# Performance work log

Hardware: AMD Instinct MI355X
Metric: run time of the kernel (lower is better)

Reference implementation:

```python
import jax, jax.numpy as jnp
import numpy as np

D_MODEL = 1024
NHEAD = 16
D_K = D_MODEL // NHEAD
MAX_REL = 1024


def setup_inputs() -> dict:
    key = jax.random.key(0)
    ks = jax.random.split(key, 6)
    B, S = 4, 2048
    s = 1.0 / np.sqrt(D_MODEL)
    x = jax.random.normal(ks[0], (B, S, D_MODEL), dtype=jnp.float32)
    W_qkv = jax.random.normal(ks[1], (D_MODEL, 3 * D_MODEL), dtype=jnp.float32) * s
    b_qkv = jnp.zeros((3 * D_MODEL,), dtype=jnp.float32)
    W_out = jax.random.normal(ks[2], (D_MODEL, D_MODEL), dtype=jnp.float32) * s
    b_out = jnp.zeros((D_MODEL,), dtype=jnp.float32)
    # torch init is zeros; use small random so bias path is exercised
    rel_bias = jax.random.normal(ks[3], (2 * MAX_REL + 1, NHEAD), dtype=jnp.float32) * 0.02
    return {"x": x, "W_qkv": W_qkv, "b_qkv": b_qkv, "W_out": W_out,
            "b_out": b_out, "rel_bias": rel_bias}


def reference(x, W_qkv, b_qkv, W_out, b_out, rel_bias):
    B, S, D = x.shape
    qkv = x @ W_qkv + b_qkv                      # [B,S,3D]
    qkv = qkv.reshape(B, S, 3, NHEAD, D_K)
    q, k, v = qkv[:, :, 0], qkv[:, :, 1], qkv[:, :, 2]  # [B,S,H,dk]
    # scores: [B,H,S,S]
    scores = jnp.einsum('bihd,bjhd->bhij', q, k) / jnp.sqrt(jnp.float32(D_K))
    idxs = jnp.arange(S)
    rel = jnp.clip(idxs[:, None] - idxs[None, :] + MAX_REL, 0, 2 * MAX_REL)  # [S,S]
    bias = rel_bias[rel]                         # [S,S,H]
    scores = scores + jnp.transpose(bias, (2, 0, 1))[None]  # broadcast over batch
    attn = jax.nn.softmax(scores, axis=-1)       # dropout p=0 (eval)
    out = jnp.einsum('bhij,bjhd->bihd', attn, v).reshape(B, S, D)
    return out @ W_out + b_out
```

## Files before the change

### kernel.cpp

```cpp
#include <hip/hip_runtime.h>

#define S_LEN 2048
#define NHEADS 16
#define DK 64
#define DMODEL 1024
#define QSCALE 0.18033688011f

typedef float f32x4 __attribute__((ext_vector_type(4)));
typedef _Float16 f16x8 __attribute__((ext_vector_type(8)));
typedef _Float16 f16x4 __attribute__((ext_vector_type(4)));
typedef __fp16 h16x2 __attribute__((ext_vector_type(2)));

__device__ __forceinline__ unsigned short f2h_bits(float f) {
  _Float16 h = (_Float16)f;
  unsigned short u; __builtin_memcpy(&u, &h, 2); return u;
}

__device__ __forceinline__ f32x4 mfma16(f16x8 a, f16x8 b, f32x4 c) {
  return __builtin_amdgcn_mfma_f32_16x16x32_f16(a, b, c, 0, 0, 0);
}
__device__ __forceinline__ f32x4 mfma16k16(f16x4 a, f16x4 b, f32x4 c) {
  return __builtin_amdgcn_mfma_f32_16x16x16f16(a, b, c, 0, 0, 0);
}
__device__ __forceinline__ f16x8 frag_ld(const unsigned short* p) {
  return *(const f16x8*)p;
}

#define GLD_LDS(g, l)                                                          \
  __builtin_amdgcn_global_load_lds(                                            \
      (const __attribute__((address_space(1))) void*)(g),                      \
      (__attribute__((address_space(3))) void*)(l), 16, 0, 0)

__global__ void convert_f32_f16(const float* __restrict__ in,
                                unsigned short* __restrict__ out, int n4) {
  int i = blockIdx.x * blockDim.x + threadIdx.x;
  if (i < n4) {
    f32x4 v = *(const f32x4*)(in + (size_t)i * 4);
    unsigned short o[4];
#pragma unroll
    for (int j = 0; j < 4; j++) o[j] = f2h_bits(v[j]);
    *(uint2*)(out + (size_t)i * 4) = *(const uint2*)o;
  }
}

__global__ void transpose_f32_f16(const float* __restrict__ in,
                                  unsigned short* __restrict__ out, int R, int C) {
  __shared__ unsigned short tile[32][33];
  int bx = blockIdx.x * 32, by = blockIdx.y * 32;
  int tx = threadIdx.x, ty = threadIdx.y;
  for (int i = ty; i < 32; i += 8)
    tile[i][tx] = f2h_bits(in[(size_t)(by + i) * C + bx + tx]);
  __syncthreads();
  for (int i = ty; i < 32; i += 8)
    out[(size_t)(bx + i) * R + by + tx] = tile[tx][i];
}

__launch_bounds__(256)
__global__ void gemm_bt(const unsigned short* __restrict__ A,
                        const unsigned short* __restrict__ Bt,
                        int M, int N, int K, int mode,
                        const float* __restrict__ bias,
                        float* __restrict__ out0,
                        unsigned short* __restrict__ q_o,
                        unsigned short* __restrict__ k_o,
                        unsigned short* __restrict__ v_o) {
  __shared__ __attribute__((aligned(16))) unsigned short As[128 * 32];
  __shared__ __attribute__((aligned(16))) unsigned short Bs[128 * 32];
  const int tid = threadIdx.x;
  const int w = tid >> 6, lane = tid & 63;
  const int wm = w >> 1, wn = w & 1;
  const int col = lane & 15, quad = lane >> 4;
  const int m0 = blockIdx.y * 128, n0 = blockIdx.x * 128;
  const f32x4 fzero = {0.f, 0.f, 0.f, 0.f};
  f32x4 acc[4][4];
#pragma unroll
  for (int i = 0; i < 4; i++)
#pragma unroll
    for (int j = 0; j < 4; j++) acc[i][j] = fzero;

  for (int k0 = 0; k0 < K; k0 += 32) {
    __syncthreads();
#pragma unroll
    for (int it = 0; it < 2; it++) {
      int c = it * 256 + tid;
      GLD_LDS(A + (size_t)(m0 + (c >> 2)) * K + k0 + (c & 3) * 8, &As[c * 8]);
      GLD_LDS(Bt + (size_t)(n0 + (c >> 2)) * K + k0 + (c & 3) * 8, &Bs[c * 8]);
    }
    __syncthreads();
    f16x8 af[4], bfr[4];
#pragma unroll
    for (int mi = 0; mi < 4; mi++)
      af[mi] = frag_ld(&As[(wm * 64 + mi * 16 + col) * 32 + quad * 8]);
#pragma unroll
    for (int ni = 0; ni < 4; ni++)
      bfr[ni] = frag_ld(&Bs[(wn * 64 + ni * 16 + col) * 32 + quad * 8]);
#pragma unroll
    for (int mi = 0; mi < 4; mi++)
#pragma unroll
      for (int ni = 0; ni < 4; ni++)
        acc[mi][ni] = mfma16(af[mi], bfr[ni], acc[mi][ni]);
  }

#pragma unroll
  for (int mi = 0; mi < 4; mi++) {
#pragma unroll
    for (int ni = 0; ni < 4; ni++) {
      int gm_b = m0 + wm * 64 + mi * 16 + quad * 4;
      int gn = n0 + wn * 64 + ni * 16 + col;
      float bv = bias[gn];
      if (mode == 1) {
#pragma unroll
        for (int r = 0; r < 4; r++)
          out0[(size_t)(gm_b + r) * N + gn] = acc[mi][ni][r] + bv;
      } else {
        int b = gm_b >> 11, s0 = gm_b & 2047;
        int t = gn >> 10, hd = gn & 1023;
        int h = hd >> 6, d = hd & 63;
        size_t bh = (size_t)(b * NHEADS + h);
        if (t == 2) {
          unsigned short o4[4];
#pragma unroll
          for (int r = 0; r < 4; r++) o4[r] = f2h_bits(acc[mi][ni][r] + bv);
          *(uint2*)&v_o[(bh * DK + d) * S_LEN + s0] = *(const uint2*)o4;
        } else {
          unsigned short* dst = (t == 0) ? q_o : k_o;
          float sc = (t == 0) ? QSCALE : 1.0f;
#pragma unroll
          for (int r = 0; r < 4; r++)
            dst[(bh * S_LEN + s0 + r) * DK + d] = f2h_bits((acc[mi][ni][r] + bv) * sc);
        }
      }
    }
  }
}

__launch_bounds__(256)
__global__ void attn_kernel(const unsigned short* __restrict__ Q,
                            const unsigned short* __restrict__ K,
                            const unsigned short* __restrict__ Vt,
                            const float* __restrict__ rel_bias,
                            unsigned short* __restrict__ ctx) {
  __shared__ __attribute__((aligned(16))) unsigned short Ks[64 * 64];
  __shared__ __attribute__((aligned(16))) unsigned short Vs[64 * 64];
  __shared__ float brev[2112];
  const int tid = threadIdx.x;
  const int w = tid >> 6, lane = tid & 63;
  const int col = lane & 15, quad = lane >> 4;
  const int c7 = col & 7;
  const int bid = blockIdx.x;
  const int xcd = bid & 7, slot = bid >> 3;
  const int bh = (slot >> 5) * 8 + xcd;
  const int qt = slot & 31;
  const int h = bh & (NHEADS - 1), b = bh >> 4;
  const unsigned short* qp = Q + (size_t)bh * S_LEN * DK;
  const unsigned short* kp = K + (size_t)bh * S_LEN * DK;
  const unsigned short* vp = Vt + (size_t)bh * DK * S_LEN;
  const f32x4 fzero = {0.f, 0.f, 0.f, 0.f};
  const f16x4 ones = {(_Float16)1.f, (_Float16)1.f, (_Float16)1.f, (_Float16)1.f};

  const int tbase = 1985 - qt * 64;
#pragma unroll
  for (int it = 0; it < 9; it++) {
    int idx = it * 256 + tid;
    if (idx < 2112) {
      int rel = 3072 - (tbase + idx);
      rel = rel < 0 ? 0 : (rel > 2048 ? 2048 : rel);
      brev[idx] = rel_bias[rel * NHEADS + h] * 1.44269504089f;
    }
  }

  const int row_base = qt * 64 + w * 16;
  f16x8 qa0 = frag_ld(qp + (size_t)(row_base + col) * DK + quad * 8);
  f16x8 qa1 = frag_ld(qp + (size_t)(row_base + col) * DK + 32 + quad * 8);

  const int tql = quad * 4 - w * 16 - col + 63;

  f32x4 o[4];
  f32x4 lacc = fzero;
#pragma unroll
  for (int ni = 0; ni < 4; ni++) o[ni] = fzero;

  for (int ck = 0; ck < S_LEN / 64; ck++) {
    const int j0 = ck * 64;
    __syncthreads();
#pragma unroll
    for (int it = 0; it < 2; it++) {
      int c = it * 256 + tid;
      int row = c >> 3, gs = c & 7, g = gs ^ (row & 7);
      GLD_LDS(kp + (size_t)(j0 + row) * DK + g * 8, &Ks[c * 8]);
      GLD_LDS(vp + (size_t)row * S_LEN + j0 + g * 8, &Vs[c * 8]);
    }
    __syncthreads();

    const float* bp = &brev[j0 + tql];
    f32x4 sc4[4];
#pragma unroll
    for (int ni = 0; ni < 4; ni++) {
      f32x4 bias4;
#pragma unroll
      for (int r = 0; r < 4; r++) bias4[r] = bp[ni * 16 + r];
      f16x8 kb0 = frag_ld(&Ks[(ni * 16 + col) * 64 + (quad ^ c7) * 8]);
      f16x8 kb1 = frag_ld(&Ks[(ni * 16 + col) * 64 + ((quad | 4) ^ c7) * 8]);
      sc4[ni] = mfma16(kb1, qa1, mfma16(kb0, qa0, bias4));
    }
    f16x4 pa[4];
#pragma unroll
    for (int ni = 0; ni < 4; ni++) {
      float p0 = __builtin_amdgcn_exp2f(sc4[ni][0]);
      float p1 = __builtin_amdgcn_exp2f(sc4[ni][1]);
      float p2 = __builtin_amdgcn_exp2f(sc4[ni][2]);
      float p3 = __builtin_amdgcn_exp2f(sc4[ni][3]);
      h16x2 lo = __builtin_amdgcn_cvt_pkrtz(p0, p1);
      h16x2 hi = __builtin_amdgcn_cvt_pkrtz(p2, p3);
      f16x4 t;
      __builtin_memcpy(&t, &lo, 4);
      __builtin_memcpy(((char*)&t) + 4, &hi, 4);
      pa[ni] = t;
    }
#pragma unroll
    for (int ni_d = 0; ni_d < 4; ni_d++) {
#pragma unroll
      for (int ni_k = 0; ni_k < 4; ni_k++) {
        int g = ni_k * 2 + (quad >> 1);
        f16x4 vb = *(const f16x4*)&Vs[(ni_d * 16 + col) * 64 + (g ^ c7) * 8 + (quad & 1) * 4];
        o[ni_d] = mfma16k16(pa[ni_k], vb, o[ni_d]);
      }
    }
#pragma unroll
    for (int ni_k = 0; ni_k < 4; ni_k++)
      lacc = mfma16k16(pa[ni_k], ones, lacc);
  }
  float inv_r[4];
#pragma unroll
  for (int r = 0; r < 4; r++) inv_r[r] = 1.0f / lacc[r];
#pragma unroll
  for (int r = 0; r < 4; r++) {
    int srow = row_base + quad * 4 + r;
#pragma unroll
    for (int ni = 0; ni < 4; ni++) {
      int d = ni * 16 + col;
      ctx[((size_t)b * S_LEN + srow) * DMODEL + h * DK + d] = f2h_bits(o[ni][r] * inv_r[r]);
    }
  }
}

extern "C" void kernel_launch(void* const* d_in, const int* in_sizes, int n_in,
                              void* d_out, int out_size, void* d_ws, size_t ws_size,
                              hipStream_t stream) {
  (void)in_sizes; (void)n_in; (void)out_size; (void)ws_size;
  const float* x        = (const float*)d_in[0];
  const float* W_qkv    = (const float*)d_in[1];
  const float* b_qkv    = (const float*)d_in[2];
  const float* W_out    = (const float*)d_in[3];
  const float* b_out    = (const float*)d_in[4];
  const float* rel_bias = (const float*)d_in[5];
  float* out = (float*)d_out;

  char* ws = (char*)d_ws;
  unsigned short* xh     = (unsigned short*)(ws + 0);
  unsigned short* ctxh   = (unsigned short*)(ws + 0);
  unsigned short* Wqkv_t = (unsigned short*)(ws + 16777216);
  unsigned short* Wout_t = (unsigned short*)(ws + 23068672);
  unsigned short* Qb     = (unsigned short*)(ws + 25165824);
  unsigned short* Kb     = (unsigned short*)(ws + 41943040);
  unsigned short* Vtb    = (unsigned short*)(ws + 58720256);

  convert_f32_f16<<<(8192 * 1024 / 4 + 255) / 256, 256, 0, stream>>>(x, xh, 8192 * 1024 / 4);
  transpose_f32_f16<<<dim3(3072 / 32, 1024 / 32), dim3(32, 8), 0, stream>>>(W_qkv, Wqkv_t, 1024, 3072);
  transpose_f32_f16<<<dim3(1024 / 32, 1024 / 32), dim3(32, 8), 0, stream>>>(W_out, Wout_t, 1024, 1024);
  gemm_bt<<<dim3(3072 / 128, 8192 / 128), 256, 0, stream>>>(
      xh, Wqkv_t, 8192, 3072, 1024, 0, b_qkv, nullptr, Qb, Kb, Vtb);
  attn_kernel<<<4 * NHEADS * (S_LEN / 64), 256, 0, stream>>>(Qb, Kb, Vtb, rel_bias, ctxh);
  gemm_bt<<<dim3(1024 / 128, 8192 / 128), 256, 0, stream>>>(
      ctxh, Wout_t, 8192, 1024, 1024, 1, b_out, out, nullptr, nullptr, nullptr);
}
```

Measured before the change: 334.7 us.

## Split attention keys across waves instead of queries, reduce partial outputs in LDS

The attention kernel now has each wave handle all 64 query rows against its own 16-key slice of every 64-key tile, instead of 16 query rows against all 64 keys. This lets each wave load one K fragment and one V fragment set per tile and reuse it across four query sub-blocks, cutting LDS fragment reads per MFMA. Row sums are now accumulated with scalar adds and a cross-lane shuffle, replacing the ones-vector MFMA. The price is a 16-tile output accumulator per thread, a launch bound requesting 3 blocks per CU, and a serialized cross-wave LDS reduction of the output at the end.

New measurement: 328.3 us. No clear change (-1.9%).

```diff
diff --git a/kernel.cpp b/kernel.cpp
--- a/kernel.cpp
+++ b/kernel.cpp
@@ -134,15 +134,19 @@
   }
 }
 
-__launch_bounds__(256)
+__launch_bounds__(256, 3)
 __global__ void attn_kernel(const unsigned short* __restrict__ Q,
                             const unsigned short* __restrict__ K,
                             const unsigned short* __restrict__ Vt,
                             const float* __restrict__ rel_bias,
                             unsigned short* __restrict__ ctx) {
-  __shared__ __attribute__((aligned(16))) unsigned short Ks[64 * 64];
-  __shared__ __attribute__((aligned(16))) unsigned short Vs[64 * 64];
-  __shared__ float brev[2112];
+  __shared__ __attribute__((aligned(16))) char smem[25088];
+  unsigned short* Ks = (unsigned short*)smem;
+  unsigned short* Vs = (unsigned short*)(smem + 8192);
+  float* brev = (float*)(smem + 16384);
+  float* lred = (float*)(smem + 24832);
+  float* red  = (float*)smem;
+
   const int tid = threadIdx.x;
   const int w = tid >> 6, lane = tid & 63;
   const int col = lane & 15, quad = lane >> 4;
@@ -156,7 +160,6 @@
   const unsigned short* kp = K + (size_t)bh * S_LEN * DK;
   const unsigned short* vp = Vt + (size_t)bh * DK * S_LEN;
   const f32x4 fzero = {0.f, 0.f, 0.f, 0.f};
-  const f16x4 ones = {(_Float16)1.f, (_Float16)1.f, (_Float16)1.f, (_Float16)1.f};
 
   const int tbase = 1985 - qt * 64;
 #pragma unroll
@@ -169,78 +172,115 @@
     }
   }
 
-  const int row_base = qt * 64 + w * 16;
-  f16x8 qa0 = frag_ld(qp + (size_t)(row_base + col) * DK + quad * 8);
-  f16x8 qa1 = frag_ld(qp + (size_t)(row_base + col) * DK + 32 + quad * 8);
-
-  const int tql = quad * 4 - w * 16 - col + 63;
-
-  f32x4 o[4];
-  f32x4 lacc = fzero;
-#pragma unroll
-  for (int ni = 0; ni < 4; ni++) o[ni] = fzero;
+  f16x8 qb[4][2];
+#pragma unroll
+  for (int qs = 0; qs < 4; qs++)
+#pragma unroll
+    for (int ks = 0; ks < 2; ks++)
+      qb[qs][ks] = frag_ld(qp + (size_t)(qt * 64 + qs * 16 + col) * DK + ks * 32 + quad * 8);
+
+  const int cA = tid, cB = 256 + tid;
+  const int rA = cA >> 3, gA = (cA & 7) ^ (rA & 7);
+  const int rB = cB >> 3, gB = (cB & 7) ^ (rB & 7);
+  const unsigned short* kgA = kp + rA * DK + gA * 8;
+  const unsigned short* kgB = kp + rB * DK + gB * 8;
+  const unsigned short* vgA = vp + (size_t)rA * S_LEN + gA * 8;
+  const unsigned short* vgB = vp + (size_t)rB * S_LEN + gB * 8;
+  unsigned short* lkA = &Ks[cA * 8];
+  unsigned short* lkB = &Ks[cB * 8];
+  unsigned short* lvA = &Vs[cA * 8];
+  unsigned short* lvB = &Vs[cB * 8];
+
+  const float* bp = &brev[w * 16 + quad * 4 - col + 15];
+
+  f32x4 o[4][4];
+  float rsum[4];
+#pragma unroll
+  for (int qs = 0; qs < 4; qs++) {
+#pragma unroll
+    for (int ds = 0; ds < 4; ds++) o[qs][ds] = fzero;
+    rsum[qs] = 0.f;
+  }
+
+  const int kaoff0 = (w * 16 + col) * 64 + (quad ^ c7) * 8;
+  const int kaoff1 = (w * 16 + col) * 64 + ((4 + quad) ^ c7) * 8;
+  const int vgrp = ((w * 2 + (quad >> 1)) ^ c7) * 8 + (quad & 1) * 4;
 
   for (int ck = 0; ck < S_LEN / 64; ck++) {
-    const int j0 = ck * 64;
-    __syncthreads();
-#pragma unroll
-    for (int it = 0; it < 2; it++) {
-      int c = it * 256 + tid;
-      int row = c >> 3, gs = c & 7, g = gs ^ (row & 7);
-      GLD_LDS(kp + (size_t)(j0 + row) * DK + g * 8, &Ks[c * 8]);
-      GLD_LDS(vp + (size_t)row * S_LEN + j0 + g * 8, &Vs[c * 8]);
-    }
-    __syncthreads();
-
-    const float* bp = &brev[j0 + tql];
-    f32x4 sc4[4];
-#pragma unroll
-    for (int ni = 0; ni < 4; ni++) {
+    __syncthreads();
+    GLD_LDS(kgA, lkA); GLD_LDS(kgB, lkB);
+    GLD_LDS(vgA, lvA); GLD_LDS(vgB, lvB);
+    __syncthreads();
+
+    f16x8 ka0 = frag_ld(&Ks[kaoff0]);
+    f16x8 ka1 = frag_ld(&Ks[kaoff1]);
+    f16x4 vb[4];
+#pragma unroll
+    for (int ds = 0; ds < 4; ds++)
+      vb[ds] = *(const f16x4*)&Vs[(ds * 16 + col) * 64 + vgrp];
+
+#pragma unroll
+    for (int qs = 0; qs < 4; qs++) {
       f32x4 bias4;
 #pragma unroll
-      for (int r = 0; r < 4; r++) bias4[r] = bp[ni * 16 + r];
-      f16x8 kb0 = frag_ld(&Ks[(ni * 16 + col) * 64 + (quad ^ c7) * 8]);
-      f16x8 kb1 = frag_ld(&Ks[(ni * 16 + col) * 64 + ((quad | 4) ^ c7) * 8]);
-      sc4[ni] = mfma16(kb1, qa1, mfma16(kb0, qa0, bias4));
-    }
-    f16x4 pa[4];
-#pragma unroll
-    for (int ni = 0; ni < 4; ni++) {
-      float p0 = __builtin_amdgcn_exp2f(sc4[ni][0]);
-      float p1 = __builtin_amdgcn_exp2f(sc4[ni][1]);
-      float p2 = __builtin_amdgcn_exp2f(sc4[ni][2]);
-      float p3 = __builtin_amdgcn_exp2f(sc4[ni][3]);
+      for (int r = 0; r < 4; r++) bias4[r] = bp[(3 - qs) * 16 + r];
+      f32x4 sc = mfma16(ka1, qb[qs][1], mfma16(ka0, qb[qs][0], bias4));
+      float p0 = __builtin_amdgcn_exp2f(sc[0]);
+      float p1 = __builtin_amdgcn_exp2f(sc[1]);
+      float p2 = __builtin_amdgcn_exp2f(sc[2]);
+      float p3 = __builtin_amdgcn_exp2f(sc[3]);
+      rsum[qs] += (p0 + p1) + (p2 + p3);
       h16x2 lo = __builtin_amdgcn_cvt_pkrtz(p0, p1);
       h16x2 hi = __builtin_amdgcn_cvt_pkrtz(p2, p3);
-      f16x4 t;
-      __builtin_memcpy(&t, &lo, 4);
-      __builtin_memcpy(((char*)&t) + 4, &hi, 4);
-      pa[ni] = t;
-    }
-#pragma unroll
-    for (int ni_d = 0; ni_d < 4; ni_d++) {
-#pragma unroll
-      for (int ni_k = 0; ni_k < 4; ni_k++) {
-        int g = ni_k * 2 + (quad >> 1);
-        f16x4 vb = *(const f16x4*)&Vs[(ni_d * 16 + col) * 64 + (g ^ c7) * 8 + (quad & 1) * 4];
-        o[ni_d] = mfma16k16(pa[ni_k], vb, o[ni_d]);
+      f16x4 pa;
+      __builtin_memcpy(&pa, &lo, 4);
+      __builtin_memcpy(((char*)&pa) + 4, &hi, 4);
+#pragma unroll
+      for (int ds = 0; ds < 4; ds++)
+        o[qs][ds] = mfma16k16(pa, vb[ds], o[qs][ds]);
+    }
+    kgA += 64 * DK; kgB += 64 * DK; vgA += 64; vgB += 64; bp += 64;
+  }
+
+#pragma unroll
+  for (int qs = 0; qs < 4; qs++) {
+    rsum[qs] += __shfl_xor(rsum[qs], 16);
+    rsum[qs] += __shfl_xor(rsum[qs], 32);
+  }
+
+  __syncthreads();
+  for (int ws = 3; ws >= 0; ws--) {
+    if (w == ws) {
+#pragma unroll
+      for (int qs = 0; qs < 4; qs++) {
+#pragma unroll
+        for (int ds = 0; ds < 4; ds++) {
+#pragma unroll
+          for (int r = 0; r < 4; r++) {
+            int q = qs * 16 + quad * 4 + r, d = ds * 16 + col;
+            if (ws == 3) red[q * 68 + d] = o[qs][ds][r];
+            else         red[q * 68 + d] += o[qs][ds][r];
+          }
+        }
+        int ql = qs * 16 + col;
+        if (ws == 3) lred[ql] = rsum[qs];
+        else         lred[ql] += rsum[qs];
       }
     }
-#pragma unroll
-    for (int ni_k = 0; ni_k < 4; ni_k++)
-      lacc = mfma16k16(pa[ni_k], ones, lacc);
-  }
-  float inv_r[4];
-#pragma unroll
-  for (int r = 0; r < 4; r++) inv_r[r] = 1.0f / lacc[r];
-#pragma unroll
-  for (int r = 0; r < 4; r++) {
-    int srow = row_base + quad * 4 + r;
-#pragma unroll
-    for (int ni = 0; ni < 4; ni++) {
-      int d = ni * 16 + col;
-      ctx[((size_t)b * S_LEN + srow) * DMODEL + h * DK + d] = f2h_bits(o[ni][r] * inv_r[r]);
-    }
+    __syncthreads();
+  }
+
+#pragma unroll
+  for (int pass = 0; pass < 4; pass++) {
+    int ql = w * 16 + pass * 4 + quad;
+    f32x4 ov = *(const f32x4*)&red[ql * 68 + col * 4];
+    float inv = 1.0f / lred[ql];
+    h16x2 lo = __builtin_amdgcn_cvt_pkrtz(ov[0] * inv, ov[1] * inv);
+    h16x2 hi = __builtin_amdgcn_cvt_pkrtz(ov[2] * inv, ov[3] * inv);
+    uint2 pkd;
+    __builtin_memcpy(&pkd.x, &lo, 4);
+    __builtin_memcpy(&pkd.y, &hi, 4);
+    *(uint2*)&ctx[((size_t)b * S_LEN + qt * 64 + ql) * DMODEL + h * DK + col * 4] = pkd;
   }
 }
 
```
